# Performance work log

Hardware: AMD Instinct MI355X
Metric: run time of the kernel (lower is better)

Reference implementation:

```python
import jax, jax.numpy as jnp
import numpy as np

N = 40000      # nodes
E = 640000     # edges (avg degree 16)
D_IN = 256     # input_size
H = 128        # hidden_size
C = 64         # num_classes
L = 2          # num_middle_layers


def spmm(val, row, col, mat):
    # sparse [N,N] @ dense [N,D]: gather neighbor rows, scale, scatter-add
    return jax.ops.segment_sum(val[:, None] * mat[col], row, num_segments=mat.shape[0])


def setup_inputs() -> dict:
    key = jax.random.key(0)
    ks = jax.random.split(key, 12)
    x = jax.random.normal(ks[0], (N, D_IN), dtype=jnp.float32)
    edge_row = jax.random.randint(ks[1], (E,), 0, N)
    edge_col = jax.random.randint(ks[2], (E,), 0, N)
    edge_val = jax.random.uniform(ks[3], (E,), dtype=jnp.float32) / 16.0  # ~normalized adjacency
    # Linear params (stored [in, out]; math equivalent to torch x @ W.T + b)
    w1 = jax.random.normal(ks[4], (D_IN, H), dtype=jnp.float32) * (1.0 / np.sqrt(D_IN))
    b1 = jax.random.normal(ks[5], (H,), dtype=jnp.float32) * 0.01
    wm = jax.random.normal(ks[6], (L, H, H), dtype=jnp.float32) * (1.0 / np.sqrt(H))
    bm = jax.random.normal(ks[7], (L, H), dtype=jnp.float32) * 0.01
    w2 = jax.random.normal(ks[8], (H, C), dtype=jnp.float32) * (1.0 / np.sqrt(H))
    b2 = jax.random.normal(ks[9], (C,), dtype=jnp.float32) * 0.01
    time_step = jnp.array(0.1, dtype=jnp.float32)
    return {"x": x, "edge_row": edge_row, "edge_col": edge_col, "edge_val": edge_val,
            "w1": w1, "b1": b1, "wm": wm, "bm": bm, "w2": w2, "b2": b2,
            "time_step": time_step}


def reference(x, edge_row, edge_col, edge_val, w1, b1, wm, bm, w2, b2, time_step):
    # dropout p=0 -> identity
    h = jax.nn.relu(spmm(edge_val, edge_row, edge_col, x @ w1 + b1))
    for i in range(L):  # residual middle layers: x <- x + relu(A @ (x W + b)) * dt
        f = jax.nn.relu(spmm(edge_val, edge_row, edge_col, h @ wm[i] + bm[i]))
        h = h + f * time_step
    return spmm(edge_val, edge_row, edge_col, h @ w2 + b2)
```

## Files before the change

kernel.cpp:

```cpp
#include <hip/hip_runtime.h>


#define DIN 256
#define HID 128
#define NCLS 64
#define VAL_DEC 1.9073486328125e-6f
#define SB 256

typedef __attribute__((ext_vector_type(8))) short bf16x8;
typedef __attribute__((ext_vector_type(4))) float f32x4;

static __device__ __forceinline__ float bf2f(unsigned int u) {
    return __uint_as_float(u << 16);
}
static __device__ __forceinline__ unsigned short f2bf(float f) {
    unsigned int i = __float_as_uint(f);
    return (unsigned short)((i + 0x7FFFu + ((i >> 16) & 1u)) >> 16);
}
static __device__ __forceinline__ unsigned int pack2(float a, float b) {
    return (unsigned int)f2bf(a) | ((unsigned int)f2bf(b) << 16);
}

__global__ __launch_bounds__(256) void prep_hist_kernel(
        const float* __restrict__ w1, const float* __restrict__ wm,
        const float* __restrict__ w2, unsigned short* __restrict__ w1t,
        unsigned short* __restrict__ wmt, unsigned short* __restrict__ w2t, int L,
        const int* __restrict__ erow, int* __restrict__ counts_t, int E, int NB) {
    __shared__ int cnt[256];
    const int tid = threadIdx.x;
    for (int k = tid; k < NB; k += 256) cnt[k] = 0;

    const int n1 = DIN * HID;
    const int n2 = n1 + L * HID * HID;
    const int n3 = n2 + HID * NCLS;
    for (int idx = blockIdx.x * 256 + tid; idx < n3; idx += SB * 256) {
        if (idx < n1) {
            int n = idx / DIN, k = idx - n * DIN;
            w1t[idx] = f2bf(w1[(size_t)k * HID + n]);
        } else if (idx < n2) {
            int j = idx - n1;
            int i = j / (HID * HID), r = j - i * (HID * HID);
            int n = r / HID, k = r - n * HID;
            wmt[j] = f2bf(wm[(size_t)i * HID * HID + (size_t)k * HID + n]);
        } else {
            int j = idx - n2;
            int n = j / HID, k = j - n * HID;
            w2t[j] = f2bf(w2[(size_t)k * NCLS + n]);
        }
    }
    __syncthreads();
    const int chunk = (E + SB - 1) / SB;
    const int lo = blockIdx.x * chunk;
    const int hi = min(lo + chunk, E);
    for (int e = lo + tid; e < hi; e += 256)
        atomicAdd(&cnt[erow[e] >> 8], 1);
    __syncthreads();
    for (int k = tid; k < NB; k += 256)
        counts_t[k * SB + blockIdx.x] = cnt[k];
}

__global__ __launch_bounds__(1024) void scan_sums_kernel(
        const int* __restrict__ a, int* __restrict__ bsums, int n) {
    __shared__ int wsum[16];
    const int lane = threadIdx.x & 63;
    const int wid  = threadIdx.x >> 6;
    int i = blockIdx.x * 1024 + threadIdx.x;
    int v = (i < n) ? a[i] : 0;
    #pragma unroll
    for (int d = 32; d >= 1; d >>= 1) v += __shfl_xor(v, d, 64);
    if (lane == 0) wsum[wid] = v;
    __syncthreads();
    if (threadIdx.x == 0) {
        int s = 0;
        #pragma unroll
        for (int w = 0; w < 16; ++w) s += wsum[w];
        bsums[blockIdx.x] = s;
    }
}

__global__ __launch_bounds__(1024) void scan_fix_kernel(
        const int* __restrict__ a, const int* __restrict__ bsums,
        int* __restrict__ out, int n, int nb) {
    __shared__ int wsum[16];
    __shared__ int bpref_s;
    const int lane = threadIdx.x & 63;
    const int wid  = threadIdx.x >> 6;
    const int b = blockIdx.x;
    if (wid == 0) {
        int v = (lane < nb && lane < b) ? bsums[lane] : 0;
        #pragma unroll
        for (int d = 32; d >= 1; d >>= 1) v += __shfl_xor(v, d, 64);
        if (lane == 0) bpref_s = v;
    }
    int i = b * 1024 + (int)threadIdx.x;
    int v = (i < n) ? a[i] : 0;
    int incl = v;
    #pragma unroll
    for (int d = 1; d < 64; d <<= 1) {
        int t = __shfl_up(incl, d, 64);
        if (lane >= d) incl += t;
    }
    if (lane == 63) wsum[wid] = incl;
    __syncthreads();
    int wpref = 0;
    #pragma unroll
    for (int w = 0; w < 16; ++w)
        if (w < wid) wpref += wsum[w];
    int excl = bpref_s + wpref + incl - v;
    if (i < n) out[i] = excl;
    if (i == n) out[n] = excl;
}

__global__ __launch_bounds__(256) void mega_kernel(
        const float* __restrict__ x, const unsigned short* __restrict__ w1t,
        const float* __restrict__ b1, unsigned short* __restrict__ z,
        const int* __restrict__ erow, const int* __restrict__ ecol,
        const float* __restrict__ eval, const int* __restrict__ starts,
        unsigned int* __restrict__ bw, unsigned char* __restrict__ br,
        int E, int NB, int gemmBlocks) {
    const int tid = threadIdx.x;
    if ((int)blockIdx.x >= gemmBlocks) {
        __shared__ int ptr[256];
        const int sb = blockIdx.x - gemmBlocks;
        for (int k = tid; k < NB; k += 256) ptr[k] = starts[k * SB + sb];
        __syncthreads();
        const int chunk = (E + SB - 1) / SB;
        const int lo = sb * chunk;
        const int hi = min(lo + chunk, E);
        for (int e = lo + tid; e < hi; e += 256) {
            int r = erow[e];
            int q = min((int)(eval[e] * 524288.0f + 0.5f), 32767);
            unsigned int w = ((unsigned int)ecol[e] << 15) | (unsigned int)q;
            int p = atomicAdd(&ptr[r >> 8], 1);
            bw[p] = w;
            br[p] = (unsigned char)(r & 255);
        }
        return;
    }
    __shared__ __align__(16) unsigned short Alds[64 * 40];
    __shared__ __align__(16) unsigned short Blds[128 * 40];
    const int bm   = blockIdx.x * 64;
    const int wave = tid >> 6;
    const int lane = tid & 63;
    const int m16  = lane & 15;
    const int quad = lane >> 4;
    const int ar = tid >> 2, ac = (tid & 3) * 8;

    f32x4 acc[8] = {};
    for (int k0 = 0; k0 < DIN; k0 += 32) {
        float4 a0 = *(const float4*)&x[(size_t)(bm + ar) * DIN + k0 + ac];
        float4 a1 = *(const float4*)&x[(size_t)(bm + ar) * DIN + k0 + ac + 4];
        uint4 av;
        av.x = pack2(a0.x, a0.y); av.y = pack2(a0.z, a0.w);
        av.z = pack2(a1.x, a1.y); av.w = pack2(a1.z, a1.w);
        *(uint4*)&Alds[ar * 40 + ac] = av;
        #pragma unroll
        for (int i = 0; i < 2; ++i) {
            int c = tid + 256 * i;
            int brow = c >> 2, bc = (c & 3) * 8;
            *(uint4*)&Blds[brow * 40 + bc] = *(const uint4*)&w1t[(size_t)brow * DIN + k0 + bc];
        }
        __syncthreads();
        bf16x8 af = *(const bf16x8*)&Alds[(wave * 16 + m16) * 40 + quad * 8];
        #pragma unroll
        for (int j = 0; j < 8; ++j) {
            bf16x8 bfr = *(const bf16x8*)&Blds[(j * 16 + m16) * 40 + quad * 8];
            acc[j] = __builtin_amdgcn_mfma_f32_16x16x32_bf16(af, bfr, acc[j], 0, 0, 0);
        }
        __syncthreads();
    }
    #pragma unroll
    for (int j = 0; j < 8; ++j) {
        int col = j * 16 + m16;
        float bb = b1[col];
        #pragma unroll
        for (int r = 0; r < 4; ++r) {
            int row = bm + wave * 16 + quad * 4 + r;
            z[(size_t)row * HID + col] = f2bf(acc[j][r] + bb);
        }
    }
}

__global__ __launch_bounds__(256) void finalize_kernel(
        const int* __restrict__ starts, const unsigned int* __restrict__ bw,
        const unsigned char* __restrict__ br, unsigned int* __restrict__ edges,
        int* __restrict__ offs, int N, int NB) {
    __shared__ int cnt[256];
    __shared__ int posl[256];
    __shared__ int ws[4];
    const int tid = threadIdx.x;
    const int k = blockIdx.x;
    const int b0 = starts[k * SB];
    const int b1 = starts[(k + 1) * SB];
    cnt[tid] = 0;
    __syncthreads();
    for (int i = b0 + tid; i < b1; i += 256)
        atomicAdd(&cnt[br[i]], 1);
    __syncthreads();
    const int lane = tid & 63, wid = tid >> 6;
    int v = cnt[tid];
    int incl = v;
    #pragma unroll
    for (int d = 1; d < 64; d <<= 1) {
        int t = __shfl_up(incl, d, 64);
        if (lane >= d) incl += t;
    }
    if (lane == 63) ws[wid] = incl;
    __syncthreads();
    int wp = 0;
    #pragma unroll
    for (int w = 0; w < 4; ++w)
        if (w < wid) wp += ws[w];
    int excl = wp + incl - v;
    int g = (k << 8) + tid;
    if (g <= N) offs[g] = b0 + excl;
    posl[tid] = b0 + excl;
    __syncthreads();
    for (int i = b0 + tid; i < b1; i += 256) {
        int r = br[i];
        unsigned int w = bw[i];
        int p = atomicAdd(&posl[r], 1);
        edges[p] = w;
    }
}

template <int BN>
__global__ __launch_bounds__(256) void gemm_mfma_kernel(
        const unsigned short* __restrict__ A, const unsigned short* __restrict__ Wt,
        const float* __restrict__ bias, unsigned short* __restrict__ C, int K) {
    constexpr int NT = BN / 16;
    __shared__ __align__(16) unsigned short Alds[64 * 40];
    __shared__ __align__(16) unsigned short Blds[BN * 40];
    const int tid  = threadIdx.x;
    const int bm   = blockIdx.x * 64;
    const int wave = tid >> 6;
    const int lane = tid & 63;
    const int m16  = lane & 15;
    const int quad = lane >> 4;
    const int ar = tid >> 2, ac = (tid & 3) * 8;

    f32x4 acc[NT] = {};
    for (int k0 = 0; k0 < K; k0 += 32) {
        uint4 av = *(const uint4*)&A[(size_t)(bm + ar) * K + k0 + ac];
        *(uint4*)&Alds[ar * 40 + ac] = av;
        #pragma unroll
        for (int i = 0; i < BN / 64; ++i) {
            int c = tid + 256 * i;
            int brow = c >> 2, bc = (c & 3) * 8;
            *(uint4*)&Blds[brow * 40 + bc] = *(const uint4*)&Wt[(size_t)brow * K + k0 + bc];
        }
        __syncthreads();
        bf16x8 af = *(const bf16x8*)&Alds[(wave * 16 + m16) * 40 + quad * 8];
        #pragma unroll
        for (int j = 0; j < NT; ++j) {
            bf16x8 bfr = *(const bf16x8*)&Blds[(j * 16 + m16) * 40 + quad * 8];
            acc[j] = __builtin_amdgcn_mfma_f32_16x16x32_bf16(af, bfr, acc[j], 0, 0, 0);
        }
        __syncthreads();
    }
    #pragma unroll
    for (int j = 0; j < NT; ++j) {
        int col = j * 16 + m16;
        float bb = bias[col];
        #pragma unroll
        for (int r = 0; r < 4; ++r) {
            int row = bm + wave * 16 + quad * 4 + r;
            C[(size_t)row * BN + col] = f2bf(acc[j][r] + bb);
        }
    }
}

template <int D, int MODE>
__global__ __launch_bounds__(256) void spmm_kernel(
        const int* __restrict__ offs, const unsigned int* __restrict__ edges,
        const unsigned short* __restrict__ z,
        float* __restrict__ out, unsigned short* __restrict__ hb,
        const float* __restrict__ dt_ptr, int n) {
    int r = (int)((blockIdx.x * blockDim.x + threadIdx.x) >> 6);
    int lane = threadIdx.x & 63;
    if (r >= n) return;
    r = __builtin_amdgcn_readfirstlane(r);
    const int s = offs[r], e = offs[r + 1];
    float acc0 = 0.f, acc1 = 0.f;
    int p = s;
    if (D == 128) {
        const unsigned int* z32 = (const unsigned int*)z;
        for (; p + 8 <= e; p += 8) {
            unsigned int ev[8], g[8];
            #pragma unroll
            for (int i = 0; i < 8; ++i) ev[i] = __builtin_nontemporal_load(edges + p + i);
            #pragma unroll
            for (int i = 0; i < 8; ++i)
                g[i] = z32[(size_t)(ev[i] >> 15) * 64 + lane];
            #pragma unroll
            for (int i = 0; i < 8; ++i) {
                float v = (float)(ev[i] & 0x7fffu) * VAL_DEC;
                acc0 = fmaf(v, bf2f(g[i] & 0xffffu), acc0);
                acc1 = fmaf(v, bf2f(g[i] >> 16), acc1);
            }
        }
        for (; p < e; ++p) {
            unsigned int ev = __builtin_nontemporal_load(edges + p);
            float v = (float)(ev & 0x7fffu) * VAL_DEC;
            unsigned int g = z32[(size_t)(ev >> 15) * 64 + lane];
            acc0 = fmaf(v, bf2f(g & 0xffffu), acc0);
            acc1 = fmaf(v, bf2f(g >> 16), acc1);
        }
        unsigned int* hbw = (unsigned int*)hb + (size_t)r * 64 + lane;
        if (MODE == 2) {
            float2 o; o.x = acc0; o.y = acc1;
            *(float2*)&out[(size_t)r * 128 + 2 * lane] = o;
        } else if (MODE == 0) {
            *hbw = pack2(fmaxf(acc0, 0.f), fmaxf(acc1, 0.f));
        } else {
            float dt = *dt_ptr;
            unsigned int cur = *hbw;
            float f0 = bf2f(cur & 0xffffu) + fmaxf(acc0, 0.f) * dt;
            float f1 = bf2f(cur >> 16)    + fmaxf(acc1, 0.f) * dt;
            *hbw = pack2(f0, f1);
        }
    } else {
        for (; p + 8 <= e; p += 8) {
            unsigned int ev[8];
            unsigned short g[8];
            #pragma unroll
            for (int i = 0; i < 8; ++i) ev[i] = __builtin_nontemporal_load(edges + p + i);
            #pragma unroll
            for (int i = 0; i < 8; ++i)
                g[i] = z[(size_t)(ev[i] >> 15) * 64 + lane];
            #pragma unroll
            for (int i = 0; i < 8; ++i)
                acc0 = fmaf((float)(ev[i] & 0x7fffu) * VAL_DEC, bf2f(g[i]), acc0);
        }
        for (; p < e; ++p) {
            unsigned int ev = __builtin_nontemporal_load(edges + p);
            acc0 = fmaf((float)(ev & 0x7fffu) * VAL_DEC,
                        bf2f((unsigned int)z[(size_t)(ev >> 15) * 64 + lane]), acc0);
        }
        out[(size_t)r * 64 + lane] = acc0;
    }
}

extern "C" void kernel_launch(void* const* d_in, const int* in_sizes, int n_in,
                              void* d_out, int out_size, void* d_ws, size_t ws_size,
                              hipStream_t stream) {
    const float* x    = (const float*)d_in[0];
    const int*   erow = (const int*)d_in[1];
    const int*   ecol = (const int*)d_in[2];
    const float* eval = (const float*)d_in[3];
    const float* w1   = (const float*)d_in[4];
    const float* b1   = (const float*)d_in[5];
    const float* wm   = (const float*)d_in[6];
    const float* bmp  = (const float*)d_in[7];
    const float* w2   = (const float*)d_in[8];
    const float* b2   = (const float*)d_in[9];
    const float* dt   = (const float*)d_in[10];

    const int N = in_sizes[0] / DIN;
    const int E = in_sizes[1];
    const int L = in_sizes[7] / HID;
    const int NB = (N + 255) >> 8;

    float* outp = (float*)d_out;

    char* ws = (char*)d_ws;
    auto carve = [&](size_t bytes) -> char* {
        char* p = ws;
        ws += (bytes + 255) & ~(size_t)255;
        return p;
    };
    int*            counts = (int*)carve((size_t)(NB * SB + 1) * 4);
    int*            starts = (int*)carve((size_t)(NB * SB + 1) * 4);
    int*            bsums  = (int*)carve(64 * 4);
    int*            offs   = (int*)carve((size_t)(N + 1) * 4);
    unsigned int*   bw     = (unsigned int*)carve((size_t)E * 4);
    unsigned char*  brr    = (unsigned char*)carve((size_t)E);
    unsigned int*   edges  = (unsigned int*)carve((size_t)E * 4);
    unsigned short* z      = (unsigned short*)carve((size_t)N * HID * 2);
    unsigned short* hb     = (unsigned short*)carve((size_t)N * HID * 2);
    unsigned short* w1t    = (unsigned short*)carve((size_t)HID * DIN * 2);
    unsigned short* wmt    = (unsigned short*)carve((size_t)L * HID * HID * 2);
    unsigned short* w2t    = (unsigned short*)carve((size_t)NCLS * HID * 2);

    const int nscan   = NB * SB;
    const int ntiles  = (nscan + 1023) / 1024;
    const int gemm_blocks = N / 64;
    const int spmm_blocks = (N + 3) / 4;

    prep_hist_kernel<<<SB, 256, 0, stream>>>(w1, wm, w2, w1t, wmt, w2t, L,
                                             erow, counts, E, NB);
    scan_sums_kernel<<<ntiles, 1024, 0, stream>>>(counts, bsums, nscan);
    scan_fix_kernel<<<ntiles, 1024, 0, stream>>>(counts, bsums, starts, nscan, ntiles);
    mega_kernel<<<gemm_blocks + SB, 256, 0, stream>>>(
        x, w1t, b1, z, erow, ecol, eval, starts, bw, brr, E, NB, gemm_blocks);
    finalize_kernel<<<NB, 256, 0, stream>>>(starts, bw, brr, edges, offs, N, NB);

    spmm_kernel<HID, 0><<<spmm_blocks, 256, 0, stream>>>(offs, edges, z, nullptr, hb, nullptr, N);

    for (int i = 0; i < L; ++i) {
        gemm_mfma_kernel<HID><<<gemm_blocks, 256, 0, stream>>>(
            hb, wmt + (size_t)i * HID * HID, bmp + (size_t)i * HID, z, HID);
        spmm_kernel<HID, 1><<<spmm_blocks, 256, 0, stream>>>(offs, edges, z, nullptr, hb, dt, N);
    }

    gemm_mfma_kernel<NCLS><<<gemm_blocks, 256, 0, stream>>>(hb, w2t, b2, z, HID);
    spmm_kernel<NCLS, 2><<<spmm_blocks, 256, 0, stream>>>(offs, edges, z, outp, nullptr, nullptr, N);
}
```

Baseline: 264.9 us.

## Build CSR with global per-row atomics and vectorize SpMM gathers

Replaces the two-level bucketed CSR construction (block histograms, bucket scatter, finalize kernel) with a per-row global atomic histogram, a direct scan into row offsets, and a direct atomic scatter into the final edge array, which removes the finalize kernel and its intermediate buffers. The SpMM kernels are rewritten so each wave gathers multiple edges at once with 16-byte loads per lane, then reduces the partial sums across lane groups with shuffles. This trades the earlier LDS-local atomics for contended global atomics, and edge order within a row becomes nondeterministic. It also adds a memset and per-iteration predicated loads.

```diff
diff --git a/kernel.cpp b/kernel.cpp
--- a/kernel.cpp
+++ b/kernel.cpp
@@ -25,11 +25,8 @@
         const float* __restrict__ w1, const float* __restrict__ wm,
         const float* __restrict__ w2, unsigned short* __restrict__ w1t,
         unsigned short* __restrict__ wmt, unsigned short* __restrict__ w2t, int L,
-        const int* __restrict__ erow, int* __restrict__ counts_t, int E, int NB) {
-    __shared__ int cnt[256];
+        const int* __restrict__ erow, int* __restrict__ counts, int E) {
     const int tid = threadIdx.x;
-    for (int k = tid; k < NB; k += 256) cnt[k] = 0;
-
     const int n1 = DIN * HID;
     const int n2 = n1 + L * HID * HID;
     const int n3 = n2 + HID * NCLS;
@@ -48,15 +45,11 @@
             w2t[j] = f2bf(w2[(size_t)k * NCLS + n]);
         }
     }
-    __syncthreads();
     const int chunk = (E + SB - 1) / SB;
     const int lo = blockIdx.x * chunk;
     const int hi = min(lo + chunk, E);
     for (int e = lo + tid; e < hi; e += 256)
-        atomicAdd(&cnt[erow[e] >> 8], 1);
-    __syncthreads();
-    for (int k = tid; k < NB; k += 256)
-        counts_t[k * SB + blockIdx.x] = cnt[k];
+        atomicAdd(&counts[erow[e]], 1);
 }
 
 __global__ __launch_bounds__(1024) void scan_sums_kernel(
@@ -80,7 +73,7 @@
 
 __global__ __launch_bounds__(1024) void scan_fix_kernel(
         const int* __restrict__ a, const int* __restrict__ bsums,
-        int* __restrict__ out, int n, int nb) {
+        int* __restrict__ offs, int* __restrict__ ptr, int n, int nb) {
     __shared__ int wsum[16];
     __shared__ int bpref_s;
     const int lane = threadIdx.x & 63;
@@ -107,23 +100,19 @@
     for (int w = 0; w < 16; ++w)
         if (w < wid) wpref += wsum[w];
     int excl = bpref_s + wpref + incl - v;
-    if (i < n) out[i] = excl;
-    if (i == n) out[n] = excl;
+    if (i < n) { offs[i] = excl; ptr[i] = excl; }
+    if (i == n) offs[n] = excl;
 }
 
 __global__ __launch_bounds__(256) void mega_kernel(
         const float* __restrict__ x, const unsigned short* __restrict__ w1t,
         const float* __restrict__ b1, unsigned short* __restrict__ z,
         const int* __restrict__ erow, const int* __restrict__ ecol,
-        const float* __restrict__ eval, const int* __restrict__ starts,
-        unsigned int* __restrict__ bw, unsigned char* __restrict__ br,
-        int E, int NB, int gemmBlocks) {
+        const float* __restrict__ eval, int* __restrict__ ptr,
+        unsigned int* __restrict__ edges, int E, int gemmBlocks) {
     const int tid = threadIdx.x;
     if ((int)blockIdx.x >= gemmBlocks) {
-        __shared__ int ptr[256];
         const int sb = blockIdx.x - gemmBlocks;
-        for (int k = tid; k < NB; k += 256) ptr[k] = starts[k * SB + sb];
-        __syncthreads();
         const int chunk = (E + SB - 1) / SB;
         const int lo = sb * chunk;
         const int hi = min(lo + chunk, E);
@@ -131,9 +120,8 @@
             int r = erow[e];
             int q = min((int)(eval[e] * 524288.0f + 0.5f), 32767);
             unsigned int w = ((unsigned int)ecol[e] << 15) | (unsigned int)q;
-            int p = atomicAdd(&ptr[r >> 8], 1);
-            bw[p] = w;
-            br[p] = (unsigned char)(r & 255);
+            int p = atomicAdd(&ptr[r], 1);
+            edges[p] = w;
         }
         return;
     }
@@ -178,49 +166,6 @@
             int row = bm + wave * 16 + quad * 4 + r;
             z[(size_t)row * HID + col] = f2bf(acc[j][r] + bb);
         }
-    }
-}
-
-__global__ __launch_bounds__(256) void finalize_kernel(
-        const int* __restrict__ starts, const unsigned int* __restrict__ bw,
-        const unsigned char* __restrict__ br, unsigned int* __restrict__ edges,
-        int* __restrict__ offs, int N, int NB) {
-    __shared__ int cnt[256];
-    __shared__ int posl[256];
-    __shared__ int ws[4];
-    const int tid = threadIdx.x;
-    const int k = blockIdx.x;
-    const int b0 = starts[k * SB];
-    const int b1 = starts[(k + 1) * SB];
-    cnt[tid] = 0;
-    __syncthreads();
-    for (int i = b0 + tid; i < b1; i += 256)
-        atomicAdd(&cnt[br[i]], 1);
-    __syncthreads();
-    const int lane = tid & 63, wid = tid >> 6;
-    int v = cnt[tid];
-    int incl = v;
-    #pragma unroll
-    for (int d = 1; d < 64; d <<= 1) {
-        int t = __shfl_up(incl, d, 64);
-        if (lane >= d) incl += t;
-    }
-    if (lane == 63) ws[wid] = incl;
-    __syncthreads();
-    int wp = 0;
-    #pragma unroll
-    for (int w = 0; w < 4; ++w)
-        if (w < wid) wp += ws[w];
-    int excl = wp + incl - v;
-    int g = (k << 8) + tid;
-    if (g <= N) offs[g] = b0 + excl;
-    posl[tid] = b0 + excl;
-    __syncthreads();
-    for (int i = b0 + tid; i < b1; i += 256) {
-        int r = br[i];
-        unsigned int w = bw[i];
-        int p = atomicAdd(&posl[r], 1);
-        edges[p] = w;
     }
 }
 
@@ -270,74 +215,109 @@
     }
 }
 
-template <int D, int MODE>
-__global__ __launch_bounds__(256) void spmm_kernel(
+template <int MODE>
+__global__ __launch_bounds__(256) void spmm128_kernel(
         const int* __restrict__ offs, const unsigned int* __restrict__ edges,
-        const unsigned short* __restrict__ z,
-        float* __restrict__ out, unsigned short* __restrict__ hb,
+        const unsigned short* __restrict__ z, unsigned short* __restrict__ hb,
         const float* __restrict__ dt_ptr, int n) {
     int r = (int)((blockIdx.x * blockDim.x + threadIdx.x) >> 6);
-    int lane = threadIdx.x & 63;
     if (r >= n) return;
     r = __builtin_amdgcn_readfirstlane(r);
+    const int lane = threadIdx.x & 63;
+    const int g = lane >> 4;
+    const int c = lane & 15;
     const int s = offs[r], e = offs[r + 1];
-    float acc0 = 0.f, acc1 = 0.f;
-    int p = s;
-    if (D == 128) {
-        const unsigned int* z32 = (const unsigned int*)z;
-        for (; p + 8 <= e; p += 8) {
-            unsigned int ev[8], g[8];
-            #pragma unroll
-            for (int i = 0; i < 8; ++i) ev[i] = __builtin_nontemporal_load(edges + p + i);
-            #pragma unroll
-            for (int i = 0; i < 8; ++i)
-                g[i] = z32[(size_t)(ev[i] >> 15) * 64 + lane];
-            #pragma unroll
-            for (int i = 0; i < 8; ++i) {
-                float v = (float)(ev[i] & 0x7fffu) * VAL_DEC;
-                acc0 = fmaf(v, bf2f(g[i] & 0xffffu), acc0);
-                acc1 = fmaf(v, bf2f(g[i] >> 16), acc1);
-            }
-        }
-        for (; p < e; ++p) {
-            unsigned int ev = __builtin_nontemporal_load(edges + p);
-            float v = (float)(ev & 0x7fffu) * VAL_DEC;
-            unsigned int g = z32[(size_t)(ev >> 15) * 64 + lane];
-            acc0 = fmaf(v, bf2f(g & 0xffffu), acc0);
-            acc1 = fmaf(v, bf2f(g >> 16), acc1);
-        }
-        unsigned int* hbw = (unsigned int*)hb + (size_t)r * 64 + lane;
-        if (MODE == 2) {
-            float2 o; o.x = acc0; o.y = acc1;
-            *(float2*)&out[(size_t)r * 128 + 2 * lane] = o;
-        } else if (MODE == 0) {
-            *hbw = pack2(fmaxf(acc0, 0.f), fmaxf(acc1, 0.f));
+    const uint4* __restrict__ z4 = (const uint4*)z;
+    float acc[8] = {0.f, 0.f, 0.f, 0.f, 0.f, 0.f, 0.f, 0.f};
+    for (int p = s; p < e; p += 8) {
+        const int p0 = p + g, p1 = p + 4 + g;
+        unsigned int ev0 = (p0 < e) ? __builtin_nontemporal_load(edges + p0) : 0u;
+        unsigned int ev1 = (p1 < e) ? __builtin_nontemporal_load(edges + p1) : 0u;
+        uint4 g0 = z4[(size_t)(ev0 >> 15) * 16 + c];
+        uint4 g1 = z4[(size_t)(ev1 >> 15) * 16 + c];
+        float v0 = (float)(ev0 & 0x7fffu) * VAL_DEC;
+        float v1 = (float)(ev1 & 0x7fffu) * VAL_DEC;
+        unsigned int wa[4] = {g0.x, g0.y, g0.z, g0.w};
+        unsigned int wb[4] = {g1.x, g1.y, g1.z, g1.w};
+        #pragma unroll
+        for (int j = 0; j < 4; ++j) {
+            acc[2 * j]     = fmaf(v0, bf2f(wa[j] & 0xffffu), acc[2 * j]);
+            acc[2 * j + 1] = fmaf(v0, bf2f(wa[j] >> 16),     acc[2 * j + 1]);
+            acc[2 * j]     = fmaf(v1, bf2f(wb[j] & 0xffffu), acc[2 * j]);
+            acc[2 * j + 1] = fmaf(v1, bf2f(wb[j] >> 16),     acc[2 * j + 1]);
+        }
+    }
+    #pragma unroll
+    for (int j = 0; j < 8; ++j) {
+        acc[j] += __shfl_xor(acc[j], 16, 64);
+        acc[j] += __shfl_xor(acc[j], 32, 64);
+    }
+    if (g == 0) {
+        uint4* hw = (uint4*)((unsigned int*)hb + (size_t)r * 64 + c * 4);
+        uint4 o;
+        if (MODE == 0) {
+            o.x = pack2(fmaxf(acc[0], 0.f), fmaxf(acc[1], 0.f));
+            o.y = pack2(fmaxf(acc[2], 0.f), fmaxf(acc[3], 0.f));
+            o.z = pack2(fmaxf(acc[4], 0.f), fmaxf(acc[5], 0.f));
+            o.w = pack2(fmaxf(acc[6], 0.f), fmaxf(acc[7], 0.f));
         } else {
-            float dt = *dt_ptr;
-            unsigned int cur = *hbw;
-            float f0 = bf2f(cur & 0xffffu) + fmaxf(acc0, 0.f) * dt;
-            float f1 = bf2f(cur >> 16)    + fmaxf(acc1, 0.f) * dt;
-            *hbw = pack2(f0, f1);
-        }
-    } else {
-        for (; p + 8 <= e; p += 8) {
-            unsigned int ev[8];
-            unsigned short g[8];
-            #pragma unroll
-            for (int i = 0; i < 8; ++i) ev[i] = __builtin_nontemporal_load(edges + p + i);
-            #pragma unroll
-            for (int i = 0; i < 8; ++i)
-                g[i] = z[(size_t)(ev[i] >> 15) * 64 + lane];
-            #pragma unroll
-            for (int i = 0; i < 8; ++i)
-                acc0 = fmaf((float)(ev[i] & 0x7fffu) * VAL_DEC, bf2f(g[i]), acc0);
-        }
-        for (; p < e; ++p) {
-            unsigned int ev = __builtin_nontemporal_load(edges + p);
-            acc0 = fmaf((float)(ev & 0x7fffu) * VAL_DEC,
-                        bf2f((unsigned int)z[(size_t)(ev >> 15) * 64 + lane]), acc0);
-        }
-        out[(size_t)r * 64 + lane] = acc0;
+            const float dt = *dt_ptr;
+            uint4 cur = *hw;
+            o.x = pack2(bf2f(cur.x & 0xffffu) + fmaxf(acc[0], 0.f) * dt,
+                        bf2f(cur.x >> 16)     + fmaxf(acc[1], 0.f) * dt);
+            o.y = pack2(bf2f(cur.y & 0xffffu) + fmaxf(acc[2], 0.f) * dt,
+                        bf2f(cur.y >> 16)     + fmaxf(acc[3], 0.f) * dt);
+            o.z = pack2(bf2f(cur.z & 0xffffu) + fmaxf(acc[4], 0.f) * dt,
+                        bf2f(cur.z >> 16)     + fmaxf(acc[5], 0.f) * dt);
+            o.w = pack2(bf2f(cur.w & 0xffffu) + fmaxf(acc[6], 0.f) * dt,
+                        bf2f(cur.w >> 16)     + fmaxf(acc[7], 0.f) * dt);
+        }
+        *hw = o;
+    }
+}
+
+__global__ __launch_bounds__(256) void spmm64_kernel(
+        const int* __restrict__ offs, const unsigned int* __restrict__ edges,
+        const unsigned short* __restrict__ z, float* __restrict__ out, int n) {
+    int r = (int)((blockIdx.x * blockDim.x + threadIdx.x) >> 6);
+    if (r >= n) return;
+    r = __builtin_amdgcn_readfirstlane(r);
+    const int lane = threadIdx.x & 63;
+    const int g = lane >> 3;
+    const int c = lane & 7;
+    const int s = offs[r], e = offs[r + 1];
+    const uint4* __restrict__ z4 = (const uint4*)z;
+    float acc[8] = {0.f, 0.f, 0.f, 0.f, 0.f, 0.f, 0.f, 0.f};
+    for (int p = s; p < e; p += 16) {
+        const int p0 = p + g, p1 = p + 8 + g;
+        unsigned int ev0 = (p0 < e) ? __builtin_nontemporal_load(edges + p0) : 0u;
+        unsigned int ev1 = (p1 < e) ? __builtin_nontemporal_load(edges + p1) : 0u;
+        uint4 g0 = z4[(size_t)(ev0 >> 15) * 8 + c];
+        uint4 g1 = z4[(size_t)(ev1 >> 15) * 8 + c];
+        float v0 = (float)(ev0 & 0x7fffu) * VAL_DEC;
+        float v1 = (float)(ev1 & 0x7fffu) * VAL_DEC;
+        unsigned int wa[4] = {g0.x, g0.y, g0.z, g0.w};
+        unsigned int wb[4] = {g1.x, g1.y, g1.z, g1.w};
+        #pragma unroll
+        for (int j = 0; j < 4; ++j) {
+            acc[2 * j]     = fmaf(v0, bf2f(wa[j] & 0xffffu), acc[2 * j]);
+            acc[2 * j + 1] = fmaf(v0, bf2f(wa[j] >> 16),     acc[2 * j + 1]);
+            acc[2 * j]     = fmaf(v1, bf2f(wb[j] & 0xffffu), acc[2 * j]);
+            acc[2 * j + 1] = fmaf(v1, bf2f(wb[j] >> 16),     acc[2 * j + 1]);
+        }
+    }
+    #pragma unroll
+    for (int j = 0; j < 8; ++j) {
+        acc[j] += __shfl_xor(acc[j], 8, 64);
+        acc[j] += __shfl_xor(acc[j], 16, 64);
+        acc[j] += __shfl_xor(acc[j], 32, 64);
+    }
+    if (g == 0) {
+        float* op = &out[(size_t)r * 64 + c * 8];
+        float4 o0 = {acc[0], acc[1], acc[2], acc[3]};
+        float4 o1 = {acc[4], acc[5], acc[6], acc[7]};
+        *(float4*)op = o0;
+        *(float4*)(op + 4) = o1;
     }
 }
 
@@ -359,7 +339,6 @@
     const int N = in_sizes[0] / DIN;
     const int E = in_sizes[1];
     const int L = in_sizes[7] / HID;
-    const int NB = (N + 255) >> 8;
 
     float* outp = (float*)d_out;
 
@@ -369,12 +348,10 @@
         ws += (bytes + 255) & ~(size_t)255;
         return p;
     };
-    int*            counts = (int*)carve((size_t)(NB * SB + 1) * 4);
-    int*            starts = (int*)carve((size_t)(NB * SB + 1) * 4);
+    int*            counts = (int*)carve((size_t)(N + 1) * 4);
+    int*            offs   = (int*)carve((size_t)(N + 1) * 4);
+    int*            ptr    = (int*)carve((size_t)(N + 1) * 4);
     int*            bsums  = (int*)carve(64 * 4);
-    int*            offs   = (int*)carve((size_t)(N + 1) * 4);
-    unsigned int*   bw     = (unsigned int*)carve((size_t)E * 4);
-    unsigned char*  brr    = (unsigned char*)carve((size_t)E);
     unsigned int*   edges  = (unsigned int*)carve((size_t)E * 4);
     unsigned short* z      = (unsigned short*)carve((size_t)N * HID * 2);
     unsigned short* hb     = (unsigned short*)carve((size_t)N * HID * 2);
@@ -382,27 +359,26 @@
     unsigned short* wmt    = (unsigned short*)carve((size_t)L * HID * HID * 2);
     unsigned short* w2t    = (unsigned short*)carve((size_t)NCLS * HID * 2);
 
-    const int nscan   = NB * SB;
-    const int ntiles  = (nscan + 1023) / 1024;
+    const int ntiles      = N / 1024 + 1;
     const int gemm_blocks = N / 64;
     const int spmm_blocks = (N + 3) / 4;
 
+    hipMemsetAsync(counts, 0, (size_t)(N + 1) * 4, stream);
     prep_hist_kernel<<<SB, 256, 0, stream>>>(w1, wm, w2, w1t, wmt, w2t, L,
-                                             erow, counts, E, NB);
-    scan_sums_kernel<<<ntiles, 1024, 0, stream>>>(counts, bsums, nscan);
-    scan_fix_kernel<<<ntiles, 1024, 0, stream>>>(counts, bsums, starts, nscan, ntiles);
+                                             erow, counts, E);
+    scan_sums_kernel<<<ntiles, 1024, 0, stream>>>(counts, bsums, N);
+    scan_fix_kernel<<<ntiles, 1024, 0, stream>>>(counts, bsums, offs, ptr, N, ntiles);
     mega_kernel<<<gemm_blocks + SB, 256, 0, stream>>>(
-        x, w1t, b1, z, erow, ecol, eval, starts, bw, brr, E, NB, gemm_blocks);
-    finalize_kernel<<<NB, 256, 0, stream>>>(starts, bw, brr, edges, offs, N, NB);
-
-    spmm_kernel<HID, 0><<<spmm_blocks, 256, 0, stream>>>(offs, edges, z, nullptr, hb, nullptr, N);
+        x, w1t, b1, z, erow, ecol, eval, ptr, edges, E, gemm_blocks);
+
+    spmm128_kernel<0><<<spmm_blocks, 256, 0, stream>>>(offs, edges, z, hb, nullptr, N);
 
     for (int i = 0; i < L; ++i) {
         gemm_mfma_kernel<HID><<<gemm_blocks, 256, 0, stream>>>(
             hb, wmt + (size_t)i * HID * HID, bmp + (size_t)i * HID, z, HID);
-        spmm_kernel<HID, 1><<<spmm_blocks, 256, 0, stream>>>(offs, edges, z, nullptr, hb, dt, N);
+        spmm128_kernel<1><<<spmm_blocks, 256, 0, stream>>>(offs, edges, z, hb, dt, N);
     }
 
     gemm_mfma_kernel<NCLS><<<gemm_blocks, 256, 0, stream>>>(hb, w2t, b2, z, HID);
-    spmm_kernel<NCLS, 2><<<spmm_blocks, 256, 0, stream>>>(offs, edges, z, outp, nullptr, nullptr, N);
-}
+    spmm64_kernel<<<spmm_blocks, 256, 0, stream>>>(offs, edges, z, outp, N);
+}
```

Measured after the change: 293.7 us. 1.11x slower.

## Store features in column-sliced layout and split SpMM across feature slices

Applied to the files above, without the earlier changes.

The intermediate feature matrices are now stored as 32-column slices, each slice contiguous across all nodes, and the GEMMs read and write this sliced layout. SpMM blocks each handle one 64-byte slice for a group of rows, and each wave processes 4 edges in parallel using 16 lanes per edge, followed by a shuffle reduction. The aim is to shrink the working set per slice so the gathers hit in L2/MALL more often, and to keep more edge gathers in flight. In exchange there are more blocks, the edge list is re-read once per slice, and each row pays a cross-lane reduction.

```diff
diff --git a/kernel.cpp b/kernel.cpp
--- a/kernel.cpp
+++ b/kernel.cpp
@@ -117,7 +117,7 @@
         const int* __restrict__ erow, const int* __restrict__ ecol,
         const float* __restrict__ eval, const int* __restrict__ starts,
         unsigned int* __restrict__ bw, unsigned char* __restrict__ br,
-        int E, int NB, int gemmBlocks) {
+        int E, int NB, int gemmBlocks, int n) {
     const int tid = threadIdx.x;
     if ((int)blockIdx.x >= gemmBlocks) {
         __shared__ int ptr[256];
@@ -176,7 +176,7 @@
         #pragma unroll
         for (int r = 0; r < 4; ++r) {
             int row = bm + wave * 16 + quad * 4 + r;
-            z[(size_t)row * HID + col] = f2bf(acc[j][r] + bb);
+            z[((size_t)(col >> 5) * n + row) * 32 + (col & 31)] = f2bf(acc[j][r] + bb);
         }
     }
 }
@@ -227,7 +227,7 @@
 template <int BN>
 __global__ __launch_bounds__(256) void gemm_mfma_kernel(
         const unsigned short* __restrict__ A, const unsigned short* __restrict__ Wt,
-        const float* __restrict__ bias, unsigned short* __restrict__ C, int K) {
+        const float* __restrict__ bias, unsigned short* __restrict__ C, int K, int n) {
     constexpr int NT = BN / 16;
     __shared__ __align__(16) unsigned short Alds[64 * 40];
     __shared__ __align__(16) unsigned short Blds[BN * 40];
@@ -241,7 +241,7 @@
 
     f32x4 acc[NT] = {};
     for (int k0 = 0; k0 < K; k0 += 32) {
-        uint4 av = *(const uint4*)&A[(size_t)(bm + ar) * K + k0 + ac];
+        uint4 av = *(const uint4*)&A[((size_t)(k0 >> 5) * n + bm + ar) * 32 + ac];
         *(uint4*)&Alds[ar * 40 + ac] = av;
         #pragma unroll
         for (int i = 0; i < BN / 64; ++i) {
@@ -265,79 +265,65 @@
         #pragma unroll
         for (int r = 0; r < 4; ++r) {
             int row = bm + wave * 16 + quad * 4 + r;
-            C[(size_t)row * BN + col] = f2bf(acc[j][r] + bb);
+            C[((size_t)(col >> 5) * n + row) * 32 + (col & 31)] = f2bf(acc[j][r] + bb);
         }
     }
 }
 
 template <int D, int MODE>
-__global__ __launch_bounds__(256) void spmm_kernel(
+__global__ __launch_bounds__(256) void spmm_sliced_kernel(
         const int* __restrict__ offs, const unsigned int* __restrict__ edges,
         const unsigned short* __restrict__ z,
         float* __restrict__ out, unsigned short* __restrict__ hb,
-        const float* __restrict__ dt_ptr, int n) {
-    int r = (int)((blockIdx.x * blockDim.x + threadIdx.x) >> 6);
-    int lane = threadIdx.x & 63;
+        const float* __restrict__ dt_ptr, int n, int rgh) {
+    const int bid = blockIdx.x;
+    const int x = bid & 7;
+    int slice, rowgrp;
+    if (D == 128) { slice = x >> 1; rowgrp = (x & 1) * rgh + (bid >> 3); }
+    else          { slice = x >> 2; rowgrp = (x & 3) * rgh + (bid >> 3); }
+    int r = rowgrp * 4 + (int)(threadIdx.x >> 6);
     if (r >= n) return;
     r = __builtin_amdgcn_readfirstlane(r);
+    const int lane = (int)threadIdx.x & 63;
+    const int g = lane >> 4;
+    const int c = lane & 15;
     const int s = offs[r], e = offs[r + 1];
+    const unsigned int* __restrict__ zs =
+        (const unsigned int*)z + (size_t)slice * n * 16;
     float acc0 = 0.f, acc1 = 0.f;
-    int p = s;
-    if (D == 128) {
-        const unsigned int* z32 = (const unsigned int*)z;
-        for (; p + 8 <= e; p += 8) {
-            unsigned int ev[8], g[8];
-            #pragma unroll
-            for (int i = 0; i < 8; ++i) ev[i] = __builtin_nontemporal_load(edges + p + i);
-            #pragma unroll
-            for (int i = 0; i < 8; ++i)
-                g[i] = z32[(size_t)(ev[i] >> 15) * 64 + lane];
-            #pragma unroll
-            for (int i = 0; i < 8; ++i) {
-                float v = (float)(ev[i] & 0x7fffu) * VAL_DEC;
-                acc0 = fmaf(v, bf2f(g[i] & 0xffffu), acc0);
-                acc1 = fmaf(v, bf2f(g[i] >> 16), acc1);
-            }
-        }
-        for (; p < e; ++p) {
-            unsigned int ev = __builtin_nontemporal_load(edges + p);
-            float v = (float)(ev & 0x7fffu) * VAL_DEC;
-            unsigned int g = z32[(size_t)(ev >> 15) * 64 + lane];
-            acc0 = fmaf(v, bf2f(g & 0xffffu), acc0);
-            acc1 = fmaf(v, bf2f(g >> 16), acc1);
-        }
-        unsigned int* hbw = (unsigned int*)hb + (size_t)r * 64 + lane;
+    for (int p = s; p < e; p += 8) {
+        const int p0 = p + g, p1 = p + 4 + g;
+        unsigned int ev0 = (p0 < e) ? __builtin_nontemporal_load(edges + p0) : 0u;
+        unsigned int ev1 = (p1 < e) ? __builtin_nontemporal_load(edges + p1) : 0u;
+        unsigned int g0 = zs[(size_t)(ev0 >> 15) * 16 + c];
+        unsigned int g1 = zs[(size_t)(ev1 >> 15) * 16 + c];
+        float v0 = (float)(ev0 & 0x7fffu) * VAL_DEC;
+        float v1 = (float)(ev1 & 0x7fffu) * VAL_DEC;
+        acc0 = fmaf(v0, bf2f(g0 & 0xffffu), acc0);
+        acc1 = fmaf(v0, bf2f(g0 >> 16),     acc1);
+        acc0 = fmaf(v1, bf2f(g1 & 0xffffu), acc0);
+        acc1 = fmaf(v1, bf2f(g1 >> 16),     acc1);
+    }
+    acc0 += __shfl_xor(acc0, 16, 64);
+    acc1 += __shfl_xor(acc1, 16, 64);
+    acc0 += __shfl_xor(acc0, 32, 64);
+    acc1 += __shfl_xor(acc1, 32, 64);
+    if (g == 0) {
         if (MODE == 2) {
             float2 o; o.x = acc0; o.y = acc1;
-            *(float2*)&out[(size_t)r * 128 + 2 * lane] = o;
-        } else if (MODE == 0) {
-            *hbw = pack2(fmaxf(acc0, 0.f), fmaxf(acc1, 0.f));
+            *(float2*)&out[(size_t)r * D + slice * 32 + c * 2] = o;
         } else {
-            float dt = *dt_ptr;
-            unsigned int cur = *hbw;
-            float f0 = bf2f(cur & 0xffffu) + fmaxf(acc0, 0.f) * dt;
-            float f1 = bf2f(cur >> 16)    + fmaxf(acc1, 0.f) * dt;
-            *hbw = pack2(f0, f1);
-        }
-    } else {
-        for (; p + 8 <= e; p += 8) {
-            unsigned int ev[8];
-            unsigned short g[8];
-            #pragma unroll
-            for (int i = 0; i < 8; ++i) ev[i] = __builtin_nontemporal_load(edges + p + i);
-            #pragma unroll
-            for (int i = 0; i < 8; ++i)
-                g[i] = z[(size_t)(ev[i] >> 15) * 64 + lane];
-            #pragma unroll
-            for (int i = 0; i < 8; ++i)
-                acc0 = fmaf((float)(ev[i] & 0x7fffu) * VAL_DEC, bf2f(g[i]), acc0);
-        }
-        for (; p < e; ++p) {
-            unsigned int ev = __builtin_nontemporal_load(edges + p);
-            acc0 = fmaf((float)(ev & 0x7fffu) * VAL_DEC,
-                        bf2f((unsigned int)z[(size_t)(ev >> 15) * 64 + lane]), acc0);
-        }
-        out[(size_t)r * 64 + lane] = acc0;
+            unsigned int* hw = (unsigned int*)hb +
+                (size_t)slice * n * 16 + (size_t)r * 16 + c;
+            if (MODE == 0) {
+                *hw = pack2(fmaxf(acc0, 0.f), fmaxf(acc1, 0.f));
+            } else {
+                const float dt = *dt_ptr;
+                unsigned int cur = *hw;
+                *hw = pack2(bf2f(cur & 0xffffu) + fmaxf(acc0, 0.f) * dt,
+                            bf2f(cur >> 16)     + fmaxf(acc1, 0.f) * dt);
+            }
+        }
     }
 }
 
@@ -385,24 +371,29 @@
     const int nscan   = NB * SB;
     const int ntiles  = (nscan + 1023) / 1024;
     const int gemm_blocks = N / 64;
-    const int spmm_blocks = (N + 3) / 4;
+    const int rg      = (N + 3) / 4;
+    const int rgh128  = (rg + 1) / 2;
+    const int rgq64   = (rg + 3) / 4;
 
     prep_hist_kernel<<<SB, 256, 0, stream>>>(w1, wm, w2, w1t, wmt, w2t, L,
                                              erow, counts, E, NB);
     scan_sums_kernel<<<ntiles, 1024, 0, stream>>>(counts, bsums, nscan);
     scan_fix_kernel<<<ntiles, 1024, 0, stream>>>(counts, bsums, starts, nscan, ntiles);
     mega_kernel<<<gemm_blocks + SB, 256, 0, stream>>>(
-        x, w1t, b1, z, erow, ecol, eval, starts, bw, brr, E, NB, gemm_blocks);
+        x, w1t, b1, z, erow, ecol, eval, starts, bw, brr, E, NB, gemm_blocks, N);
     finalize_kernel<<<NB, 256, 0, stream>>>(starts, bw, brr, edges, offs, N, NB);
 
-    spmm_kernel<HID, 0><<<spmm_blocks, 256, 0, stream>>>(offs, edges, z, nullptr, hb, nullptr, N);
+    spmm_sliced_kernel<HID, 0><<<rgh128 * 8, 256, 0, stream>>>(
+        offs, edges, z, nullptr, hb, nullptr, N, rgh128);
 
     for (int i = 0; i < L; ++i) {
         gemm_mfma_kernel<HID><<<gemm_blocks, 256, 0, stream>>>(
-            hb, wmt + (size_t)i * HID * HID, bmp + (size_t)i * HID, z, HID);
-        spmm_kernel<HID, 1><<<spmm_blocks, 256, 0, stream>>>(offs, edges, z, nullptr, hb, dt, N);
-    }
-
-    gemm_mfma_kernel<NCLS><<<gemm_blocks, 256, 0, stream>>>(hb, w2t, b2, z, HID);
-    spmm_kernel<NCLS, 2><<<spmm_blocks, 256, 0, stream>>>(offs, edges, z, outp, nullptr, nullptr, N);
-}
+            hb, wmt + (size_t)i * HID * HID, bmp + (size_t)i * HID, z, HID, N);
+        spmm_sliced_kernel<HID, 1><<<rgh128 * 8, 256, 0, stream>>>(
+            offs, edges, z, nullptr, hb, dt, N, rgh128);
+    }
+
+    gemm_mfma_kernel<NCLS><<<gemm_blocks, 256, 0, stream>>>(hb, w2t, b2, z, HID, N);
+    spmm_sliced_kernel<NCLS, 2><<<rgq64 * 8, 256, 0, stream>>>(
+        offs, edges, z, outp, nullptr, nullptr, N, rgq64);
+}
```

Result: slower. 376.2 us (+42.0%).

## Bucket edges by column range into phases for cache-local SpMM gathers

Applied to the files above, without the earlier changes.

Edges are re-sorted by a composite key (column bucket, row), which gives eight phases, each touching only one eighth of the source rows. Each wave handles ten rows and walks all phases, with a block-wide barrier between phases, so the gathered z working set stays in cache. Half-waves handle alternate edges and are combined with a shuffle. The cost is a larger histogram, scan and offsets array (8N entries), extra per-row offset loads and barriers, and lower parallelism with ten rows per wave.

```diff
diff --git a/kernel.cpp b/kernel.cpp
--- a/kernel.cpp
+++ b/kernel.cpp
@@ -6,6 +6,8 @@
 #define NCLS 64
 #define VAL_DEC 1.9073486328125e-6f
 #define SB 256
+#define NPH 8
+#define RPW 10
 
 typedef __attribute__((ext_vector_type(8))) short bf16x8;
 typedef __attribute__((ext_vector_type(4))) float f32x4;
@@ -25,8 +27,9 @@
         const float* __restrict__ w1, const float* __restrict__ wm,
         const float* __restrict__ w2, unsigned short* __restrict__ w1t,
         unsigned short* __restrict__ wmt, unsigned short* __restrict__ w2t, int L,
-        const int* __restrict__ erow, int* __restrict__ counts_t, int E, int NB) {
-    __shared__ int cnt[256];
+        const int* __restrict__ erow, const int* __restrict__ ecol,
+        int* __restrict__ counts_t, int E, int NB, int RQ, int N) {
+    __shared__ int cnt[1280];
     const int tid = threadIdx.x;
     for (int k = tid; k < NB; k += 256) cnt[k] = 0;
 
@@ -52,8 +55,10 @@
     const int chunk = (E + SB - 1) / SB;
     const int lo = blockIdx.x * chunk;
     const int hi = min(lo + chunk, E);
-    for (int e = lo + tid; e < hi; e += 256)
-        atomicAdd(&cnt[erow[e] >> 8], 1);
+    for (int e = lo + tid; e < hi; e += 256) {
+        int key = (int)((unsigned)ecol[e] / (unsigned)RQ) * N + erow[e];
+        atomicAdd(&cnt[key >> 8], 1);
+    }
     __syncthreads();
     for (int k = tid; k < NB; k += 256)
         counts_t[k * SB + blockIdx.x] = cnt[k];
@@ -87,7 +92,8 @@
     const int wid  = threadIdx.x >> 6;
     const int b = blockIdx.x;
     if (wid == 0) {
-        int v = (lane < nb && lane < b) ? bsums[lane] : 0;
+        int v = 0;
+        for (int j = lane; j < b; j += 64) v += bsums[j];
         #pragma unroll
         for (int d = 32; d >= 1; d >>= 1) v += __shfl_xor(v, d, 64);
         if (lane == 0) bpref_s = v;
@@ -117,10 +123,10 @@
         const int* __restrict__ erow, const int* __restrict__ ecol,
         const float* __restrict__ eval, const int* __restrict__ starts,
         unsigned int* __restrict__ bw, unsigned char* __restrict__ br,
-        int E, int NB, int gemmBlocks) {
+        int E, int NB, int gemmBlocks, int RQ, int N) {
     const int tid = threadIdx.x;
     if ((int)blockIdx.x >= gemmBlocks) {
-        __shared__ int ptr[256];
+        __shared__ int ptr[1280];
         const int sb = blockIdx.x - gemmBlocks;
         for (int k = tid; k < NB; k += 256) ptr[k] = starts[k * SB + sb];
         __syncthreads();
@@ -129,11 +135,13 @@
         const int hi = min(lo + chunk, E);
         for (int e = lo + tid; e < hi; e += 256) {
             int r = erow[e];
+            int col = ecol[e];
+            int key = (int)((unsigned)col / (unsigned)RQ) * N + r;
             int q = min((int)(eval[e] * 524288.0f + 0.5f), 32767);
-            unsigned int w = ((unsigned int)ecol[e] << 15) | (unsigned int)q;
-            int p = atomicAdd(&ptr[r >> 8], 1);
+            unsigned int w = ((unsigned int)col << 15) | (unsigned int)q;
+            int p = atomicAdd(&ptr[key >> 8], 1);
             bw[p] = w;
-            br[p] = (unsigned char)(r & 255);
+            br[p] = (unsigned char)(key & 255);
         }
         return;
     }
@@ -184,7 +192,7 @@
 __global__ __launch_bounds__(256) void finalize_kernel(
         const int* __restrict__ starts, const unsigned int* __restrict__ bw,
         const unsigned char* __restrict__ br, unsigned int* __restrict__ edges,
-        int* __restrict__ offs, int N, int NB) {
+        int* __restrict__ offs2, int KN, int NB) {
     __shared__ int cnt[256];
     __shared__ int posl[256];
     __shared__ int ws[4];
@@ -213,7 +221,8 @@
         if (w < wid) wp += ws[w];
     int excl = wp + incl - v;
     int g = (k << 8) + tid;
-    if (g <= N) offs[g] = b0 + excl;
+    offs2[g] = b0 + excl;
+    if (k == NB - 1 && tid == 255) offs2[KN] = b1;
     posl[tid] = b0 + excl;
     __syncthreads();
     for (int i = b0 + tid; i < b1; i += 256) {
@@ -270,74 +279,105 @@
     }
 }
 
-template <int D, int MODE>
-__global__ __launch_bounds__(256) void spmm_kernel(
-        const int* __restrict__ offs, const unsigned int* __restrict__ edges,
-        const unsigned short* __restrict__ z,
-        float* __restrict__ out, unsigned short* __restrict__ hb,
+template <int MODE>
+__global__ __launch_bounds__(256) void spmm_phased128_kernel(
+        const int* __restrict__ offs2, const unsigned int* __restrict__ edges,
+        const unsigned short* __restrict__ z, unsigned short* __restrict__ hb,
         const float* __restrict__ dt_ptr, int n) {
-    int r = (int)((blockIdx.x * blockDim.x + threadIdx.x) >> 6);
-    int lane = threadIdx.x & 63;
-    if (r >= n) return;
-    r = __builtin_amdgcn_readfirstlane(r);
-    const int s = offs[r], e = offs[r + 1];
-    float acc0 = 0.f, acc1 = 0.f;
-    int p = s;
-    if (D == 128) {
-        const unsigned int* z32 = (const unsigned int*)z;
-        for (; p + 8 <= e; p += 8) {
-            unsigned int ev[8], g[8];
-            #pragma unroll
-            for (int i = 0; i < 8; ++i) ev[i] = __builtin_nontemporal_load(edges + p + i);
-            #pragma unroll
-            for (int i = 0; i < 8; ++i)
-                g[i] = z32[(size_t)(ev[i] >> 15) * 64 + lane];
-            #pragma unroll
-            for (int i = 0; i < 8; ++i) {
-                float v = (float)(ev[i] & 0x7fffu) * VAL_DEC;
-                acc0 = fmaf(v, bf2f(g[i] & 0xffffu), acc0);
-                acc1 = fmaf(v, bf2f(g[i] >> 16), acc1);
+    const int w    = blockIdx.x * 4 + (threadIdx.x >> 6);
+    const int lane = threadIdx.x & 63;
+    const int half = lane >> 5;
+    const int c    = lane & 31;
+    const int base = __builtin_amdgcn_readfirstlane(w * RPW);
+    const uint2* __restrict__ z2 = (const uint2*)z;
+    float acc[RPW][4] = {};
+    for (int ph = 0; ph < NPH; ++ph) {
+        const int* __restrict__ o = offs2 + (size_t)ph * n;
+        #pragma unroll
+        for (int i = 0; i < RPW; ++i) {
+            int r = base + i;
+            if (r < n) {
+                const int s = o[r], e = o[r + 1];
+                for (int p = s; p < e; p += 2) {
+                    int pp = p + half;
+                    unsigned int ev = (pp < e) ? __builtin_nontemporal_load(edges + pp) : 0u;
+                    uint2 g = z2[(size_t)(ev >> 15) * 32 + c];
+                    float v = (float)(ev & 0x7fffu) * VAL_DEC;
+                    acc[i][0] = fmaf(v, bf2f(g.x & 0xffffu), acc[i][0]);
+                    acc[i][1] = fmaf(v, bf2f(g.x >> 16),     acc[i][1]);
+                    acc[i][2] = fmaf(v, bf2f(g.y & 0xffffu), acc[i][2]);
+                    acc[i][3] = fmaf(v, bf2f(g.y >> 16),     acc[i][3]);
+                }
             }
         }
-        for (; p < e; ++p) {
-            unsigned int ev = __builtin_nontemporal_load(edges + p);
-            float v = (float)(ev & 0x7fffu) * VAL_DEC;
-            unsigned int g = z32[(size_t)(ev >> 15) * 64 + lane];
-            acc0 = fmaf(v, bf2f(g & 0xffffu), acc0);
-            acc1 = fmaf(v, bf2f(g >> 16), acc1);
-        }
-        unsigned int* hbw = (unsigned int*)hb + (size_t)r * 64 + lane;
-        if (MODE == 2) {
-            float2 o; o.x = acc0; o.y = acc1;
-            *(float2*)&out[(size_t)r * 128 + 2 * lane] = o;
-        } else if (MODE == 0) {
-            *hbw = pack2(fmaxf(acc0, 0.f), fmaxf(acc1, 0.f));
-        } else {
-            float dt = *dt_ptr;
-            unsigned int cur = *hbw;
-            float f0 = bf2f(cur & 0xffffu) + fmaxf(acc0, 0.f) * dt;
-            float f1 = bf2f(cur >> 16)    + fmaxf(acc1, 0.f) * dt;
-            *hbw = pack2(f0, f1);
-        }
-    } else {
-        for (; p + 8 <= e; p += 8) {
-            unsigned int ev[8];
-            unsigned short g[8];
-            #pragma unroll
-            for (int i = 0; i < 8; ++i) ev[i] = __builtin_nontemporal_load(edges + p + i);
-            #pragma unroll
-            for (int i = 0; i < 8; ++i)
-                g[i] = z[(size_t)(ev[i] >> 15) * 64 + lane];
-            #pragma unroll
-            for (int i = 0; i < 8; ++i)
-                acc0 = fmaf((float)(ev[i] & 0x7fffu) * VAL_DEC, bf2f(g[i]), acc0);
-        }
-        for (; p < e; ++p) {
-            unsigned int ev = __builtin_nontemporal_load(edges + p);
-            acc0 = fmaf((float)(ev & 0x7fffu) * VAL_DEC,
-                        bf2f((unsigned int)z[(size_t)(ev >> 15) * 64 + lane]), acc0);
-        }
-        out[(size_t)r * 64 + lane] = acc0;
+        __syncthreads();
+    }
+    const float dt = (MODE == 1) ? *dt_ptr : 0.f;
+    #pragma unroll
+    for (int i = 0; i < RPW; ++i) {
+        int r = base + i;
+        if (r >= n) continue;
+        float a0 = acc[i][0] + __shfl_xor(acc[i][0], 32, 64);
+        float a1 = acc[i][1] + __shfl_xor(acc[i][1], 32, 64);
+        float a2 = acc[i][2] + __shfl_xor(acc[i][2], 32, 64);
+        float a3 = acc[i][3] + __shfl_xor(acc[i][3], 32, 64);
+        if (half == 0) {
+            uint2* hw = (uint2*)hb + (size_t)r * 32 + c;
+            uint2 o;
+            if (MODE == 0) {
+                o.x = pack2(fmaxf(a0, 0.f), fmaxf(a1, 0.f));
+                o.y = pack2(fmaxf(a2, 0.f), fmaxf(a3, 0.f));
+            } else {
+                uint2 cur = *hw;
+                o.x = pack2(bf2f(cur.x & 0xffffu) + fmaxf(a0, 0.f) * dt,
+                            bf2f(cur.x >> 16)     + fmaxf(a1, 0.f) * dt);
+                o.y = pack2(bf2f(cur.y & 0xffffu) + fmaxf(a2, 0.f) * dt,
+                            bf2f(cur.y >> 16)     + fmaxf(a3, 0.f) * dt);
+            }
+            *hw = o;
+        }
+    }
+}
+
+__global__ __launch_bounds__(256) void spmm_phased64_kernel(
+        const int* __restrict__ offs2, const unsigned int* __restrict__ edges,
+        const unsigned short* __restrict__ z, float* __restrict__ out, int n) {
+    const int w    = blockIdx.x * 4 + (threadIdx.x >> 6);
+    const int lane = threadIdx.x & 63;
+    const int half = lane >> 5;
+    const int c    = lane & 31;
+    const int base = __builtin_amdgcn_readfirstlane(w * RPW);
+    const unsigned int* __restrict__ z1 = (const unsigned int*)z;
+    float acc[RPW][2] = {};
+    for (int ph = 0; ph < NPH; ++ph) {
+        const int* __restrict__ o = offs2 + (size_t)ph * n;
+        #pragma unroll
+        for (int i = 0; i < RPW; ++i) {
+            int r = base + i;
+            if (r < n) {
+                const int s = o[r], e = o[r + 1];
+                for (int p = s; p < e; p += 2) {
+                    int pp = p + half;
+                    unsigned int ev = (pp < e) ? __builtin_nontemporal_load(edges + pp) : 0u;
+                    unsigned int g = z1[(size_t)(ev >> 15) * 32 + c];
+                    float v = (float)(ev & 0x7fffu) * VAL_DEC;
+                    acc[i][0] = fmaf(v, bf2f(g & 0xffffu), acc[i][0]);
+                    acc[i][1] = fmaf(v, bf2f(g >> 16),     acc[i][1]);
+                }
+            }
+        }
+        __syncthreads();
+    }
+    #pragma unroll
+    for (int i = 0; i < RPW; ++i) {
+        int r = base + i;
+        if (r >= n) continue;
+        float a0 = acc[i][0] + __shfl_xor(acc[i][0], 32, 64);
+        float a1 = acc[i][1] + __shfl_xor(acc[i][1], 32, 64);
+        if (half == 0) {
+            float2 o; o.x = a0; o.y = a1;
+            *(float2*)&out[(size_t)r * 64 + c * 2] = o;
+        }
     }
 }
 
@@ -356,10 +396,12 @@
     const float* b2   = (const float*)d_in[9];
     const float* dt   = (const float*)d_in[10];
 
-    const int N = in_sizes[0] / DIN;
-    const int E = in_sizes[1];
-    const int L = in_sizes[7] / HID;
-    const int NB = (N + 255) >> 8;
+    const int N  = in_sizes[0] / DIN;
+    const int E  = in_sizes[1];
+    const int L  = in_sizes[7] / HID;
+    const int RQ = (N + NPH - 1) / NPH;
+    const int KN = NPH * N;
+    const int NB = (KN + 255) >> 8;
 
     float* outp = (float*)d_out;
 
@@ -371,8 +413,8 @@
     };
     int*            counts = (int*)carve((size_t)(NB * SB + 1) * 4);
     int*            starts = (int*)carve((size_t)(NB * SB + 1) * 4);
-    int*            bsums  = (int*)carve(64 * 4);
-    int*            offs   = (int*)carve((size_t)(N + 1) * 4);
+    int*            bsums  = (int*)carve(512 * 4);
+    int*            offs2  = (int*)carve((size_t)(KN + 1) * 4);
     unsigned int*   bw     = (unsigned int*)carve((size_t)E * 4);
     unsigned char*  brr    = (unsigned char*)carve((size_t)E);
     unsigned int*   edges  = (unsigned int*)carve((size_t)E * 4);
@@ -385,24 +427,26 @@
     const int nscan   = NB * SB;
     const int ntiles  = (nscan + 1023) / 1024;
     const int gemm_blocks = N / 64;
-    const int spmm_blocks = (N + 3) / 4;
+    const int spmm_blocks = (N + 4 * RPW - 1) / (4 * RPW);
 
     prep_hist_kernel<<<SB, 256, 0, stream>>>(w1, wm, w2, w1t, wmt, w2t, L,
-                                             erow, counts, E, NB);
+                                             erow, ecol, counts, E, NB, RQ, N);
     scan_sums_kernel<<<ntiles, 1024, 0, stream>>>(counts, bsums, nscan);
     scan_fix_kernel<<<ntiles, 1024, 0, stream>>>(counts, bsums, starts, nscan, ntiles);
     mega_kernel<<<gemm_blocks + SB, 256, 0, stream>>>(
-        x, w1t, b1, z, erow, ecol, eval, starts, bw, brr, E, NB, gemm_blocks);
-    finalize_kernel<<<NB, 256, 0, stream>>>(starts, bw, brr, edges, offs, N, NB);
-
-    spmm_kernel<HID, 0><<<spmm_blocks, 256, 0, stream>>>(offs, edges, z, nullptr, hb, nullptr, N);
+        x, w1t, b1, z, erow, ecol, eval, starts, bw, brr, E, NB, gemm_blocks, RQ, N);
+    finalize_kernel<<<NB, 256, 0, stream>>>(starts, bw, brr, edges, offs2, KN, NB);
+
+    spmm_phased128_kernel<0><<<spmm_blocks, 256, 0, stream>>>(
+        offs2, edges, z, hb, nullptr, N);
 
     for (int i = 0; i < L; ++i) {
         gemm_mfma_kernel<HID><<<gemm_blocks, 256, 0, stream>>>(
             hb, wmt + (size_t)i * HID * HID, bmp + (size_t)i * HID, z, HID);
-        spmm_kernel<HID, 1><<<spmm_blocks, 256, 0, stream>>>(offs, edges, z, nullptr, hb, dt, N);
+        spmm_phased128_kernel<1><<<spmm_blocks, 256, 0, stream>>>(
+            offs2, edges, z, hb, dt, N);
     }
 
     gemm_mfma_kernel<NCLS><<<gemm_blocks, 256, 0, stream>>>(hb, w2t, b2, z, HID);
-    spmm_kernel<NCLS, 2><<<spmm_blocks, 256, 0, stream>>>(offs, edges, z, outp, nullptr, nullptr, N);
-}
+    spmm_phased64_kernel<<<spmm_blocks, 256, 0, stream>>>(offs2, edges, z, outp, N);
+}
```

New measurement: 522.8 us. 1.97x slower.
